# Kernel tuning notes

Measured on AMD Instinct MI355X. Metric: run time of the kernel, lower is better.

## Reference

```python
import jax, jax.numpy as jnp
import numpy as np
from jax.scipy.linalg import expm

N_MODES, N_LAYERS, CUTOFF, BATCH = 6, 6, 3, 1024
M2 = N_MODES * (N_MODES - 1) // 2                  # beamsplitter thetas per interferometer
N_IF = N_MODES * (N_MODES - 1) + (N_MODES - 1)     # interferometer param count = 35

_np_a = np.diag(np.sqrt(np.arange(1, CUTOFF)), 1)  # truncated annihilation operator
A = jnp.asarray(_np_a, jnp.complex64)
AD = A.conj().T
NVEC = jnp.arange(CUTOFF, dtype=jnp.float32)       # number operator diagonal
X_OP = A + AD                                      # x quadrature (hbar=2, PennyLane/SF convention)
BS_GEN = jnp.kron(AD, A) - jnp.kron(A, AD)         # Beamsplitter(theta, 0) generator
SQ_GEN = A @ A - AD @ AD                           # Squeezing(r, 0) generator (times r/2)
D_GEN = AD - A                                     # Displacement(r, 0) generator

def disp_gate(r):
    return expm(r.astype(jnp.complex64) * D_GEN)

def sq_gate(r):
    return expm(0.5 * r.astype(jnp.complex64) * SQ_GEN)

def bs_gate(theta):
    return expm(theta.astype(jnp.complex64) * BS_GEN)

def apply_1(psi, U, m):
    # psi: (B, D, ..., D); apply DxD gate U on mode m
    psi = jnp.moveaxis(psi, 1 + m, -1)
    psi = psi @ U.T
    return jnp.moveaxis(psi, -1, 1 + m)

def apply_1_batched(psi, U, m):
    # U: (B, D, D) per-sample gate (data-encoding displacement)
    psi = jnp.moveaxis(psi, 1 + m, -1)
    psi = jnp.einsum('b...j,bij->b...i', psi, U)
    return jnp.moveaxis(psi, -1, 1 + m)

def apply_2(psi, U, m):
    psi = jnp.moveaxis(psi, (1 + m, 2 + m), (-2, -1))
    sh = psi.shape
    psi = (psi.reshape(sh[:-2] + (CUTOFF * CUTOFF,)) @ U.T).reshape(sh)
    return jnp.moveaxis(psi, (-2, -1), (1 + m, 2 + m))

def apply_diag(psi, d, m):
    shape = [1] * psi.ndim
    shape[1 + m] = CUTOFF
    return psi * d.reshape(shape)

def interferometer(psi, params):
    theta = params[:M2]
    rphi = params[-N_MODES:]  # faithful to source: overlaps last (unused) phi param
    n = 0
    for l in range(N_MODES):
        for k in range(N_MODES - 1):
            if (l + k) % 2 != 1:
                psi = apply_2(psi, bs_gate(theta[n]), k)
                n += 1
    for i in range(max(1, N_MODES - 1)):
        psi = apply_diag(psi, jnp.exp(1j * rphi[i] * NVEC), i)
    return psi

def cv_forward(x, theta_1, theta_2, squeezing_r, displacement_r, kerr_params):
    B = x.shape[0]
    psi = jnp.zeros((B,) + (CUTOFF,) * N_MODES, jnp.complex64)
    psi = psi.at[(slice(None),) + (0,) * N_MODES].set(1.0)  # |0...0> vacuum
    for m in range(N_MODES):  # data-encoding displacements, per-sample gates
        psi = apply_1_batched(psi, jax.vmap(disp_gate)(x[:, m]), m)
    for L in range(N_LAYERS):
        psi = interferometer(psi, theta_1[L])
        for m in range(N_MODES):
            psi = apply_1(psi, sq_gate(squeezing_r[L, m] * 0.5), m)
        psi = interferometer(psi, theta_2[L])
        for m in range(N_MODES):
            psi = apply_1(psi, disp_gate(displacement_r[L, m]), m)
            psi = apply_diag(psi, jnp.exp(1j * (kerr_params[L, m] * 0.001) * NVEC * NVEC), m)
    sum_axes = tuple(range(1, psi.ndim))
    outs = [jnp.sum(jnp.conj(psi) * apply_1(psi, X_OP, m), axis=sum_axes).real
            for m in range(N_MODES)]
    return jnp.stack(outs, axis=1)  # (B, N_MODES)

def setup_inputs() -> dict:
    key = jax.random.key(0)
    ks = jax.random.split(key, 6)
    passive_sd = 0.01 * np.pi
    return {
        'x': jax.random.normal(ks[0], (BATCH, N_MODES), jnp.float32),
        'theta_1': jax.random.normal(ks[1], (N_LAYERS, N_IF), jnp.float32) * passive_sd,
        'theta_2': jax.random.normal(ks[2], (N_LAYERS, N_IF), jnp.float32) * np.float32(0.2 * np.pi),
        'squeezing_r': jax.random.normal(ks[3], (N_LAYERS, N_MODES), jnp.float32) * 1e-3,
        'displacement_r': jax.random.normal(ks[4], (N_LAYERS, N_MODES), jnp.float32) * 1e-3,
        'kerr_params': jax.random.normal(ks[5], (N_LAYERS, N_MODES), jnp.float32) * 1e-3,
    }

def reference(x, theta_1, theta_2, squeezing_r, displacement_r, kerr_params):
    return cv_forward(x, theta_1, theta_2, squeezing_r, displacement_r, kerr_params)
```

## Files before the change

kernel.cpp:

```cpp
#include <hip/hip_runtime.h>

#define SQRT2f 1.41421356237309515f
#define SQRT3f 1.73205080756887729f

__device__ __forceinline__ float2 cmul(float2 a, float2 b) {
  return make_float2(a.x*b.x - a.y*b.y, a.x*b.y + a.y*b.x);
}
__device__ __forceinline__ float2 cadd(float2 a, float2 b) {
  return make_float2(a.x + b.x, a.y + b.y);
}

__device__ __forceinline__ void bs_q(float2* q, float c, float s,
                                     float c2, float s2, float cc, float ss,
                                     float rcs) {
  float2 a1=q[1], a3=q[3], a2=q[2], a4=q[4], a6=q[6], a5=q[5], a7=q[7];
  q[1] = make_float2(c*a1.x - s*a3.x, c*a1.y - s*a3.y);
  q[3] = make_float2(s*a1.x + c*a3.x, s*a1.y + c*a3.y);
  q[2] = make_float2(cc*a2.x - rcs*a4.x + ss*a6.x, cc*a2.y - rcs*a4.y + ss*a6.y);
  q[4] = make_float2(rcs*a2.x + c2*a4.x - rcs*a6.x, rcs*a2.y + c2*a4.y - rcs*a6.y);
  q[6] = make_float2(ss*a2.x + rcs*a4.x + cc*a6.x, ss*a2.y + rcs*a4.y + cc*a6.y);
  q[5] = make_float2(c2*a5.x - s2*a7.x, c2*a5.y - s2*a7.y);
  q[7] = make_float2(s2*a5.x + c2*a7.x, s2*a5.y + c2*a7.y);
}

template<int SP>
__device__ __forceinline__ void bs_nonet(float2* __restrict__ psi, int base,
                                         float2 cs) {
  const float c = cs.x, s = cs.y;
  const float c2 = c*c - s*s, s2 = 2.f*c*s;
  const float cc = c*c, ss = s*s, rcs = SQRT2f*c*s;
  float2 a1 = psi[base+SP],   a3 = psi[base+3*SP];
  float2 a2 = psi[base+2*SP], a4 = psi[base+4*SP], a6 = psi[base+6*SP];
  float2 a5 = psi[base+5*SP], a7 = psi[base+7*SP];
  psi[base+SP]   = make_float2(c*a1.x - s*a3.x, c*a1.y - s*a3.y);
  psi[base+3*SP] = make_float2(s*a1.x + c*a3.x, s*a1.y + c*a3.y);
  psi[base+2*SP] = make_float2(cc*a2.x - rcs*a4.x + ss*a6.x,
                               cc*a2.y - rcs*a4.y + ss*a6.y);
  psi[base+4*SP] = make_float2(rcs*a2.x + c2*a4.x - rcs*a6.x,
                               rcs*a2.y + c2*a4.y - rcs*a6.y);
  psi[base+6*SP] = make_float2(ss*a2.x + rcs*a4.x + cc*a6.x,
                               ss*a2.y + rcs*a4.y + cc*a6.y);
  psi[base+5*SP] = make_float2(c2*a5.x - s2*a7.x, c2*a5.y - s2*a7.y);
  psi[base+7*SP] = make_float2(s2*a5.x + c2*a7.x, s2*a5.y + c2*a7.y);
}

template<int SP>
__device__ __forceinline__ void sqbs_nonet(float2* __restrict__ psi, int base,
                                           const float2* __restrict__ G,
                                           float2 cs) {
  const float c = cs.x, s = cs.y;
  const float c2 = c*c - s*s, s2 = 2.f*c*s;
  const float cc = c*c, ss = s*s, rcs = SQRT2f*c*s;
  float2 A00=G[0],A02=G[1],A11=G[2],A20=G[3],A22=G[4];
  float2 B00=G[5],B02=G[6],B11=G[7],B20=G[8],B22=G[9];
  float2 v[3][3];
#pragma unroll
  for (int j = 0; j < 3; ++j)
#pragma unroll
    for (int jb = 0; jb < 3; ++jb) v[j][jb] = psi[base + j*3*SP + jb*SP];
  float2 q[9];
  {
    float2 t[3][3];
#pragma unroll
    for (int j = 0; j < 3; ++j) {
      t[j][0] = cadd(cmul(B00,v[j][0]), cmul(B02,v[j][2]));
      t[j][1] = cmul(B11,v[j][1]);
      t[j][2] = cadd(cmul(B20,v[j][0]), cmul(B22,v[j][2]));
    }
#pragma unroll
    for (int ib = 0; ib < 3; ++ib) {
      q[ib]   = cadd(cmul(A00,t[0][ib]), cmul(A02,t[2][ib]));
      q[3+ib] = cmul(A11,t[1][ib]);
      q[6+ib] = cadd(cmul(A20,t[0][ib]), cmul(A22,t[2][ib]));
    }
  }
  bs_q(q, c, s, c2, s2, cc, ss, rcs);
#pragma unroll
  for (int i = 0; i < 9; ++i) psi[base + (i/3)*3*SP + (i%3)*SP] = q[i];
}

template<int SP>
__device__ __forceinline__ void dpbs_nonet(float2* __restrict__ psi, int base,
                                           const float2* __restrict__ G,
                                           float2 cs) {
  const float c = cs.x, s = cs.y;
  const float c2 = c*c - s*s, s2 = 2.f*c*s;
  const float cc = c*c, ss = s*s, rcs = SQRT2f*c*s;
  const float2* A = G; const float2* B = G + 9;
  float2 v[3][3];
#pragma unroll
  for (int j = 0; j < 3; ++j)
#pragma unroll
    for (int jb = 0; jb < 3; ++jb) v[j][jb] = psi[base + j*3*SP + jb*SP];
  float2 q[9];
  {
    float2 t[3][3];
#pragma unroll
    for (int j = 0; j < 3; ++j)
#pragma unroll
      for (int ib = 0; ib < 3; ++ib)
        t[j][ib] = cadd(cadd(cmul(B[ib*3+0],v[j][0]), cmul(B[ib*3+1],v[j][1])),
                        cmul(B[ib*3+2],v[j][2]));
#pragma unroll
    for (int i = 0; i < 3; ++i)
#pragma unroll
      for (int ib = 0; ib < 3; ++ib)
        q[i*3+ib] = cadd(cadd(cmul(A[i*3+0],t[0][ib]), cmul(A[i*3+1],t[1][ib])),
                         cmul(A[i*3+2],t[2][ib]));
  }
  bs_q(q, c, s, c2, s2, cc, ss, rcs);
#pragma unroll
  for (int i = 0; i < 9; ++i) psi[base + (i/3)*3*SP + (i%3)*SP] = q[i];
}

template<int ST, int FOLD>
__device__ __forceinline__ void cube_sweep(float2* __restrict__ psi, int base,
                                           const float2* __restrict__ G,
                                           float2 csM, float2 csH) {
  float2 v[27];
#pragma unroll
  for (int r = 0; r < 27; ++r) v[r] = psi[base + ST*r];
  if (FOLD == 1) {
    float2 A00=G[0],A02=G[1],A11=G[2],A20=G[3],A22=G[4];
    float2 B00=G[5],B02=G[6],B11=G[7],B20=G[8],B22=G[9];
#pragma unroll
    for (int t = 0; t < 9; ++t) {
      float2 u0=v[t*3], u2=v[t*3+2];
      v[t*3]   = cadd(cmul(B00,u0), cmul(B02,u2));
      v[t*3+1] = cmul(B11, v[t*3+1]);
      v[t*3+2] = cadd(cmul(B20,u0), cmul(B22,u2));
    }
#pragma unroll
    for (int h = 0; h < 3; ++h)
#pragma unroll
      for (int lo = 0; lo < 3; ++lo) {
        int rb = h*9 + lo;
        float2 u0=v[rb], u2=v[rb+6];
        v[rb]   = cadd(cmul(A00,u0), cmul(A02,u2));
        v[rb+3] = cmul(A11, v[rb+3]);
        v[rb+6] = cadd(cmul(A20,u0), cmul(A22,u2));
      }
  }
  if (FOLD == 2) {
#pragma unroll
    for (int t = 0; t < 9; ++t) {
      float2 u0=v[t*3], u1=v[t*3+1], u2=v[t*3+2];
      v[t*3]   = cadd(cadd(cmul(G[9+0],u0),cmul(G[9+1],u1)),cmul(G[9+2],u2));
      v[t*3+1] = cadd(cadd(cmul(G[9+3],u0),cmul(G[9+4],u1)),cmul(G[9+5],u2));
      v[t*3+2] = cadd(cadd(cmul(G[9+6],u0),cmul(G[9+7],u1)),cmul(G[9+8],u2));
    }
#pragma unroll
    for (int h = 0; h < 3; ++h)
#pragma unroll
      for (int lo = 0; lo < 3; ++lo) {
        int rb = h*9 + lo;
        float2 u0=v[rb], u1=v[rb+3], u2=v[rb+6];
        v[rb]   = cadd(cadd(cmul(G[0],u0),cmul(G[1],u1)),cmul(G[2],u2));
        v[rb+3] = cadd(cadd(cmul(G[3],u0),cmul(G[4],u1)),cmul(G[5],u2));
        v[rb+6] = cadd(cadd(cmul(G[6],u0),cmul(G[7],u1)),cmul(G[8],u2));
      }
  }
  {
    const float c=csM.x, s=csM.y;
    const float c2=c*c-s*s, s2=2.f*c*s, cc=c*c, ss=s*s, rcs=SQRT2f*c*s;
#pragma unroll
    for (int h = 0; h < 3; ++h) bs_q(&v[h*9], c, s, c2, s2, cc, ss, rcs);
  }
  {
    const float c=csH.x, s=csH.y;
    const float c2=c*c-s*s, s2=2.f*c*s, cc=c*c, ss=s*s, rcs=SQRT2f*c*s;
#pragma unroll
    for (int lo = 0; lo < 3; ++lo) {
      float2 q[9];
#pragma unroll
      for (int j = 0; j < 9; ++j) q[j] = v[(j/3)*9 + (j%3)*3 + lo];
      bs_q(q, c, s, c2, s2, cc, ss, rcs);
#pragma unroll
      for (int j = 0; j < 9; ++j) v[(j/3)*9 + (j%3)*3 + lo] = q[j];
    }
  }
#pragma unroll
  for (int r = 0; r < 27; ++r) psi[base + ST*r] = v[r];
}

#define BASE5(g, s0,s1,s2,s3,s4) ({ int _d=(g); int _b=(_d%3)*(s0); _d/=3; \
  _b += (_d%3)*(s1); _d/=3; _b += (_d%3)*(s2); _d/=3; _b += (_d%3)*(s3); _d/=3; \
  _b += (_d%3)*(s4); _b; })

__device__ __forceinline__ float2 dpk_entry(const float* __restrict__ dr,
                                            const float* __restrict__ th2,
                                            const float* __restrict__ kp,
                                            int L, int mode, int i, int j) {
  float sn, cn; sincosf(SQRT3f*dr[L*6+mode], &sn, &cn);
  float sw = sn*(1.f/SQRT3f), cw = (1.f-cn)*(1.f/3.f);
  float U;
  if      (i==0) U = (j==0) ? (1.f-cw)     : (j==1) ? (-sw)         : (SQRT2f*cw);
  else if (i==1) U = (j==0) ? (sw)         : (j==1) ? (1.f-3.f*cw)  : (-SQRT2f*sw);
  else           U = (j==0) ? (SQRT2f*cw)  : (j==1) ? (SQRT2f*sw)   : (1.f-2.f*cw);
  float2 ph = make_float2(1.f, 0.f);
  if (mode < 5) { float ps, pc; sincosf(th2[L*35+29+mode], &ps, &pc);
                  ph = make_float2(pc, ps); }
  float2 phj = (j==0) ? make_float2(1.f,0.f) : (j==1) ? ph : cmul(ph, ph);
  float ks, kc; sincosf(0.001f*kp[L*6+mode], &ks, &kc);
  float2 k1 = make_float2(kc, ks);
  float2 ki = (i==0) ? make_float2(1.f,0.f)
            : (i==1) ? k1 : cmul(cmul(k1,k1), cmul(k1,k1));
  float2 t = cmul(phj, ki);
  return make_float2(U*t.x, U*t.y);
}

__global__ __launch_bounds__(128)
void cvnn_kernel(const float* __restrict__ x,
                 const float* __restrict__ th1,
                 const float* __restrict__ th2,
                 const float* __restrict__ sr,
                 const float* __restrict__ dr,
                 const float* __restrict__ kp,
                 float* __restrict__ out) {
  __shared__ float2 psi[729];
  __shared__ float2 gtab[690];
  __shared__ float red[12];

  const int tid = threadIdx.x;
  const int bidx = blockIdx.x;

  for (int f = tid; f < 690; f += 128) {
    float sn, cn; float2 v;
    if (f < 180) {
      int Lp = f/15, pos = f%15;
      int L = Lp/2, pass = Lp%2;
      float th = (pass ? th2 : th1)[L*35 + pos];
      sincosf(th, &sn, &cn); v = make_float2(cn, sn);
    } else if (f < 360) {
      int i = f - 180; int Lc = i/10, e = i%10;
      int L = Lc/3, c3 = Lc%3;
      int mode = 2*c3 + (e >= 5); int ee = e%5;
      float Sq, Cq; sincosf(0.25f*SQRT2f*sr[L*6+mode], &Sq, &Cq);
      float2 ph = make_float2(1.f, 0.f);
      if (mode < 5) { float ps, pc; sincosf(th1[L*35+29+mode], &ps, &pc);
                      ph = make_float2(pc, ps); }
      float2 ph2 = cmul(ph, ph);
      if      (ee == 0) v = make_float2(Cq, 0.f);
      else if (ee == 1) v = make_float2(Sq*ph2.x, Sq*ph2.y);
      else if (ee == 2) v = ph;
      else if (ee == 3) v = make_float2(-Sq, 0.f);
      else              v = make_float2(Cq*ph2.x, Cq*ph2.y);
    } else if (f < 630) {
      int i = f - 360; int Ld = i/18, e = i%18;
      int Ls = Ld/3, c3 = Ld%3;
      int mode = 2*c3 + (e >= 9); int ee = e%9;
      v = dpk_entry(dr, th2, kp, Ls, mode, ee/3, ee%3);
    } else if (f < 684) {
      int i = f - 630; int m = i/9, e = i%9;
      int ii = e/3, jj = e%3;
      float2 D0i = dpk_entry(dr, th2, kp, 5, m, 0, ii);
      float2 D1i = dpk_entry(dr, th2, kp, 5, m, 1, ii);
      float2 D2i = dpk_entry(dr, th2, kp, 5, m, 2, ii);
      float2 D0j = dpk_entry(dr, th2, kp, 5, m, 0, jj);
      float2 D1j = dpk_entry(dr, th2, kp, 5, m, 1, jj);
      float2 D2j = dpk_entry(dr, th2, kp, 5, m, 2, jj);
      float2 c0 = make_float2(D0i.x, -D0i.y);
      float2 c1 = make_float2(D1i.x, -D1i.y);
      float2 c2 = make_float2(D2i.x, -D2i.y);
      float2 acc = cmul(c0, D1j);
      float2 tmp = make_float2(D0j.x + SQRT2f*D2j.x, D0j.y + SQRT2f*D2j.y);
      acc = cadd(acc, cmul(c1, tmp));
      acc = cadd(acc, cmul(c2, make_float2(SQRT2f*D1j.x, SQRT2f*D1j.y)));
      v = acc;
    } else {
      int mode = f - 684;
      sincosf(SQRT3f*x[bidx*6 + mode], &sn, &cn);
      v = make_float2(sn*(1.f/SQRT3f), (1.f-cn)*(1.f/3.f));
    }
    gtab[f] = v;
  }
  __syncthreads();

  for (int idx = tid; idx < 729; idx += 128) {
    float pr = 1.f; int d = idx;
#pragma unroll
    for (int mm = 5; mm >= 0; --mm) {
      int n = d % 3; d /= 3;
      float2 dc = gtab[684 + mm];
      pr *= (n==0) ? (1.f-dc.y) : (n==1) ? dc.x : SQRT2f*dc.y;
    }
    psi[idx] = make_float2(pr, 0.f);
  }

  const int g = (tid < 81) ? tid : 0;
  const int b0 = g;
  const int h = (tid < 27) ? tid : 0;
  const int n0h = h/9, hm = (h%9)/3, hl = h%3;
  const int base123 = n0h*243 + hm*3 + hl;
  const int base345 = n0h*243 + hm*81 + hl*27;
  __syncthreads();

#define W81_BS(GI)      { if (tid < 81) bs_nonet<81>(psi, b0, gtab[GI]); \
    __syncthreads(); }
#define W81_SQBS(GS,GI) { if (tid < 81) sqbs_nonet<81>(psi, b0, &gtab[GS], gtab[GI]); \
    __syncthreads(); }
#define W81_DPBS(GD,GI) { if (tid < 81) dpbs_nonet<81>(psi, b0, &gtab[GD], gtab[GI]); \
    __syncthreads(); }
#define W27_123(F,GP,GI1,GI2) { if (tid < 27) \
    cube_sweep<9,F>(psi, base123, GP, gtab[GI1], gtab[GI2]); __syncthreads(); }
#define W27_345(F,GP,GI1,GI2) { if (tid < 27) \
    cube_sweep<1,F>(psi, base345, GP, gtab[GI1], gtab[GI2]); __syncthreads(); }

#pragma unroll
  for (int L = 0; L < 6; ++L) {
    {
      const int PB = (L*2)*15;
      if (L == 0) {
        W81_BS(PB+0);
        W27_123(0, (const float2*)nullptr, PB+1, PB+3);
        W27_345(0, (const float2*)nullptr, PB+2, PB+4);
      } else {
        const int gd = 360 + (L-1)*54;
        W81_DPBS(gd+0, PB+0);
        W27_123(2, &gtab[gd+18], PB+1, PB+3);
        W27_345(2, &gtab[gd+36], PB+2, PB+4);
      }
      W81_BS(PB+5);
      W27_123(0, (const float2*)nullptr, PB+6, PB+8);
      W27_345(0, (const float2*)nullptr, PB+7, PB+9);
      W81_BS(PB+10);
      W27_123(0, (const float2*)nullptr, PB+11, PB+13);
      W27_345(0, (const float2*)nullptr, PB+12, PB+14);
    }
    {
      const int PB = (L*2+1)*15, gs = 180 + L*30;
      W81_SQBS(gs+0, PB+0);
      W27_123(1, &gtab[gs+10], PB+1, PB+3);
      W27_345(1, &gtab[gs+20], PB+2, PB+4);
      W81_BS(PB+5);
      W27_123(0, (const float2*)nullptr, PB+6, PB+8);
      W27_345(0, (const float2*)nullptr, PB+7, PB+9);
      W81_BS(PB+10);
      W27_123(0, (const float2*)nullptr, PB+11, PB+13);
      W27_345(0, (const float2*)nullptr, PB+12, PB+14);
    }
  }

  float xs[6] = {0.f,0.f,0.f,0.f,0.f,0.f};
  for (int it = 0; it < 2; ++it) {
    int t = tid + (it << 7);
    if (t < 243) {
#define XACC(m, SS, BB) { int b_ = (BB); \
      const float2* M_ = &gtab[630 + (m)*9]; \
      float d0 = M_[0].x, d1 = M_[4].x, d2 = M_[8].x; \
      float2 M01 = M_[1], M02 = M_[2], M12 = M_[5]; \
      float2 a_ = psi[b_]; float2 e_ = psi[b_+(SS)]; float2 f_ = psi[b_+2*(SS)]; \
      xs[m] += d0*(a_.x*a_.x + a_.y*a_.y) + d1*(e_.x*e_.x + e_.y*e_.y) \
             + d2*(f_.x*f_.x + f_.y*f_.y) \
        + 2.f*(M01.x*(a_.x*e_.x + a_.y*e_.y) - M01.y*(a_.x*e_.y - a_.y*e_.x)) \
        + 2.f*(M02.x*(a_.x*f_.x + a_.y*f_.y) - M02.y*(a_.x*f_.y - a_.y*f_.x)) \
        + 2.f*(M12.x*(e_.x*f_.x + e_.y*f_.y) - M12.y*(e_.x*f_.y - e_.y*f_.x)); }
      XACC(0, 243, BASE5(t, 1, 3, 9, 27, 81));
      XACC(1, 81,  BASE5(t, 1, 3, 9, 27, 243));
      XACC(2, 27,  BASE5(t, 1, 3, 9, 81, 243));
      XACC(3, 9,   BASE5(t, 1, 3, 27, 81, 243));
      XACC(4, 3,   BASE5(t, 1, 9, 27, 81, 243));
      XACC(5, 1,   BASE5(t, 3, 9, 27, 81, 243));
    }
  }
  const int lane = tid & 63, wid = tid >> 6;
#pragma unroll
  for (int m = 0; m < 6; ++m) {
    float v = xs[m];
    for (int off = 32; off > 0; off >>= 1) v += __shfl_down(v, off);
    if (lane == 0) red[wid*6 + m] = v;
  }
  __syncthreads();
  if (tid < 6) out[bidx*6 + tid] = red[tid] + red[6 + tid];
}

extern "C" void kernel_launch(void* const* d_in, const int* in_sizes, int n_in,
                              void* d_out, int out_size, void* d_ws, size_t ws_size,
                              hipStream_t stream) {
  const float* x  = (const float*)d_in[0];
  const float* t1 = (const float*)d_in[1];
  const float* t2 = (const float*)d_in[2];
  const float* sr = (const float*)d_in[3];
  const float* dr = (const float*)d_in[4];
  const float* kp = (const float*)d_in[5];
  const int B = in_sizes[0] / 6;
  cvnn_kernel<<<B, 128, 0, stream>>>(x, t1, t2, sr, dr, kp, (float*)d_out);
}
```

Baseline: 109.1 us.

## Split cube sweeps across 81 threads with cross-lane shuffles for the third mode

Each 27-element cube sweep, previously done by 27 threads each holding 27 amplitudes, is now split so that 81 threads each hold 9 amplitudes. The second beamsplitter's mode axis is exchanged between lane triples with __shfl instead of staying within one thread. This raises the parallelism in these phases and cuts per-thread register pressure and serial work. In exchange it adds shuffle traffic and spreads the active lanes over two wavefronts, with the cube index mapping done by lane arithmetic.

```diff
diff --git a/kernel.cpp b/kernel.cpp
--- a/kernel.cpp
+++ b/kernel.cpp
@@ -10,9 +10,10 @@
   return make_float2(a.x + b.x, a.y + b.y);
 }
 
-__device__ __forceinline__ void bs_q(float2* q, float c, float s,
-                                     float c2, float s2, float cc, float ss,
-                                     float rcs) {
+__device__ __forceinline__ void bs_q(float2* q, float2 cs) {
+  const float c = cs.x, s = cs.y;
+  const float c2 = c*c - s*s, s2 = 2.f*c*s;
+  const float cc = c*c, ss = s*s, rcs = SQRT2f*c*s;
   float2 a1=q[1], a3=q[3], a2=q[2], a4=q[4], a6=q[6], a5=q[5], a7=q[7];
   q[1] = make_float2(c*a1.x - s*a3.x, c*a1.y - s*a3.y);
   q[3] = make_float2(s*a1.x + c*a3.x, s*a1.y + c*a3.y);
@@ -48,9 +49,6 @@
 __device__ __forceinline__ void sqbs_nonet(float2* __restrict__ psi, int base,
                                            const float2* __restrict__ G,
                                            float2 cs) {
-  const float c = cs.x, s = cs.y;
-  const float c2 = c*c - s*s, s2 = 2.f*c*s;
-  const float cc = c*c, ss = s*s, rcs = SQRT2f*c*s;
   float2 A00=G[0],A02=G[1],A11=G[2],A20=G[3],A22=G[4];
   float2 B00=G[5],B02=G[6],B11=G[7],B20=G[8],B22=G[9];
   float2 v[3][3];
@@ -74,7 +72,7 @@
       q[6+ib] = cadd(cmul(A20,t[0][ib]), cmul(A22,t[2][ib]));
     }
   }
-  bs_q(q, c, s, c2, s2, cc, ss, rcs);
+  bs_q(q, cs);
 #pragma unroll
   for (int i = 0; i < 9; ++i) psi[base + (i/3)*3*SP + (i%3)*SP] = q[i];
 }
@@ -83,9 +81,6 @@
 __device__ __forceinline__ void dpbs_nonet(float2* __restrict__ psi, int base,
                                            const float2* __restrict__ G,
                                            float2 cs) {
-  const float c = cs.x, s = cs.y;
-  const float c2 = c*c - s*s, s2 = 2.f*c*s;
-  const float cc = c*c, ss = s*s, rcs = SQRT2f*c*s;
   const float2* A = G; const float2* B = G + 9;
   float2 v[3][3];
 #pragma unroll
@@ -108,79 +103,78 @@
         q[i*3+ib] = cadd(cadd(cmul(A[i*3+0],t[0][ib]), cmul(A[i*3+1],t[1][ib])),
                          cmul(A[i*3+2],t[2][ib]));
   }
-  bs_q(q, c, s, c2, s2, cc, ss, rcs);
+  bs_q(q, cs);
 #pragma unroll
   for (int i = 0; i < 9; ++i) psi[base + (i/3)*3*SP + (i%3)*SP] = q[i];
 }
 
-template<int ST, int FOLD>
-__device__ __forceinline__ void cube_sweep(float2* __restrict__ psi, int base,
-                                           const float2* __restrict__ G,
-                                           float2 csM, float2 csH) {
-  float2 v[27];
-#pragma unroll
-  for (int r = 0; r < 27; ++r) v[r] = psi[base + ST*r];
+template<int FOLD, int SH, int SM, int SL>
+__device__ __forceinline__ void cube81(float2* __restrict__ psi, int base,
+                                       int h, int lb3,
+                                       const float2* __restrict__ G,
+                                       float2 csM, float2 csH) {
+  float2 v[9];
+#pragma unroll
+  for (int m = 0; m < 3; ++m)
+#pragma unroll
+    for (int l = 0; l < 3; ++l) v[m*3+l] = psi[base + h*SH + m*SM + l*SL];
   if (FOLD == 1) {
     float2 A00=G[0],A02=G[1],A11=G[2],A20=G[3],A22=G[4];
     float2 B00=G[5],B02=G[6],B11=G[7],B20=G[8],B22=G[9];
 #pragma unroll
-    for (int t = 0; t < 9; ++t) {
-      float2 u0=v[t*3], u2=v[t*3+2];
-      v[t*3]   = cadd(cmul(B00,u0), cmul(B02,u2));
-      v[t*3+1] = cmul(B11, v[t*3+1]);
-      v[t*3+2] = cadd(cmul(B20,u0), cmul(B22,u2));
-    }
-#pragma unroll
-    for (int h = 0; h < 3; ++h)
-#pragma unroll
-      for (int lo = 0; lo < 3; ++lo) {
-        int rb = h*9 + lo;
-        float2 u0=v[rb], u2=v[rb+6];
-        v[rb]   = cadd(cmul(A00,u0), cmul(A02,u2));
-        v[rb+3] = cmul(A11, v[rb+3]);
-        v[rb+6] = cadd(cmul(A20,u0), cmul(A22,u2));
-      }
+    for (int m = 0; m < 3; ++m) {
+      float2 u0=v[m*3], u2=v[m*3+2];
+      v[m*3]   = cadd(cmul(B00,u0), cmul(B02,u2));
+      v[m*3+1] = cmul(B11, v[m*3+1]);
+      v[m*3+2] = cadd(cmul(B20,u0), cmul(B22,u2));
+    }
+#pragma unroll
+    for (int l = 0; l < 3; ++l) {
+      float2 u0=v[l], u2=v[6+l];
+      v[l]   = cadd(cmul(A00,u0), cmul(A02,u2));
+      v[3+l] = cmul(A11, v[3+l]);
+      v[6+l] = cadd(cmul(A20,u0), cmul(A22,u2));
+    }
   }
   if (FOLD == 2) {
 #pragma unroll
-    for (int t = 0; t < 9; ++t) {
-      float2 u0=v[t*3], u1=v[t*3+1], u2=v[t*3+2];
-      v[t*3]   = cadd(cadd(cmul(G[9+0],u0),cmul(G[9+1],u1)),cmul(G[9+2],u2));
-      v[t*3+1] = cadd(cadd(cmul(G[9+3],u0),cmul(G[9+4],u1)),cmul(G[9+5],u2));
-      v[t*3+2] = cadd(cadd(cmul(G[9+6],u0),cmul(G[9+7],u1)),cmul(G[9+8],u2));
-    }
-#pragma unroll
-    for (int h = 0; h < 3; ++h)
-#pragma unroll
-      for (int lo = 0; lo < 3; ++lo) {
-        int rb = h*9 + lo;
-        float2 u0=v[rb], u1=v[rb+3], u2=v[rb+6];
-        v[rb]   = cadd(cadd(cmul(G[0],u0),cmul(G[1],u1)),cmul(G[2],u2));
-        v[rb+3] = cadd(cadd(cmul(G[3],u0),cmul(G[4],u1)),cmul(G[5],u2));
-        v[rb+6] = cadd(cadd(cmul(G[6],u0),cmul(G[7],u1)),cmul(G[8],u2));
-      }
-  }
-  {
-    const float c=csM.x, s=csM.y;
-    const float c2=c*c-s*s, s2=2.f*c*s, cc=c*c, ss=s*s, rcs=SQRT2f*c*s;
-#pragma unroll
-    for (int h = 0; h < 3; ++h) bs_q(&v[h*9], c, s, c2, s2, cc, ss, rcs);
-  }
-  {
-    const float c=csH.x, s=csH.y;
-    const float c2=c*c-s*s, s2=2.f*c*s, cc=c*c, ss=s*s, rcs=SQRT2f*c*s;
-#pragma unroll
-    for (int lo = 0; lo < 3; ++lo) {
-      float2 q[9];
-#pragma unroll
-      for (int j = 0; j < 9; ++j) q[j] = v[(j/3)*9 + (j%3)*3 + lo];
-      bs_q(q, c, s, c2, s2, cc, ss, rcs);
-#pragma unroll
-      for (int j = 0; j < 9; ++j) v[(j/3)*9 + (j%3)*3 + lo] = q[j];
-    }
-  }
-#pragma unroll
-  for (int r = 0; r < 27; ++r) psi[base + ST*r] = v[r];
+    for (int m = 0; m < 3; ++m) {
+      float2 u0=v[m*3], u1=v[m*3+1], u2=v[m*3+2];
+      v[m*3]   = cadd(cadd(cmul(G[9+0],u0),cmul(G[9+1],u1)),cmul(G[9+2],u2));
+      v[m*3+1] = cadd(cadd(cmul(G[9+3],u0),cmul(G[9+4],u1)),cmul(G[9+5],u2));
+      v[m*3+2] = cadd(cadd(cmul(G[9+6],u0),cmul(G[9+7],u1)),cmul(G[9+8],u2));
+    }
+#pragma unroll
+    for (int l = 0; l < 3; ++l) {
+      float2 u0=v[l], u1=v[3+l], u2=v[6+l];
+      v[l]   = cadd(cadd(cmul(G[0],u0),cmul(G[1],u1)),cmul(G[2],u2));
+      v[3+l] = cadd(cadd(cmul(G[3],u0),cmul(G[4],u1)),cmul(G[5],u2));
+      v[6+l] = cadd(cadd(cmul(G[6],u0),cmul(G[7],u1)),cmul(G[8],u2));
+    }
+  }
+  bs_q(v, csM);
+  const int hp1 = (h==2) ? 0 : h+1;
+  const int hp2 = (h==0) ? 2 : h-1;
+  const int l1 = lb3 + hp1, l2 = lb3 + hp2;
+  float2 a[9];
+#pragma unroll
+  for (int m = 0; m < 3; ++m) {
+    float2 own = (h==0) ? v[3*m]   : (h==1) ? v[3*m+1] : v[3*m+2];
+    float2 e1  = (h==0) ? v[3*m+2] : (h==1) ? v[3*m]   : v[3*m+1];
+    float2 e2  = (h==0) ? v[3*m+1] : (h==1) ? v[3*m+2] : v[3*m];
+    float2 r1, r2;
+    r1.x = __shfl(e1.x, l1, 64); r1.y = __shfl(e1.y, l1, 64);
+    r2.x = __shfl(e2.x, l2, 64); r2.y = __shfl(e2.y, l2, 64);
+    a[0+m] = (h==0) ? own : (h==2) ? r1 : r2;
+    a[3+m] = (h==1) ? own : (h==0) ? r1 : r2;
+    a[6+m] = (h==2) ? own : (h==1) ? r1 : r2;
+  }
+  bs_q(a, csH);
+#pragma unroll
+  for (int hi = 0; hi < 3; ++hi)
+#pragma unroll
+    for (int m = 0; m < 3; ++m)
+      psi[base + hi*SH + m*SM + h*SL] = a[3*hi+m];
 }
 
 #define BASE5(g, s0,s1,s2,s3,s4) ({ int _d=(g); int _b=(_d%3)*(s0); _d/=3; \
@@ -289,10 +283,15 @@
 
   const int g = (tid < 81) ? tid : 0;
   const int b0 = g;
-  const int h = (tid < 27) ? tid : 0;
-  const int n0h = h/9, hm = (h%9)/3, hl = h%3;
-  const int base123 = n0h*243 + hm*3 + hl;
-  const int base345 = n0h*243 + hm*81 + hl*27;
+  const int lane = tid & 63, wv = tid >> 6;
+  const bool cact = (wv == 0) ? (lane < 63) : (lane < 18);
+  const int lc = lane / 3;
+  const int cc = (wv == 0) ? lc : (21 + lc);
+  const int ch = lane % 3;
+  const int lb3 = lc * 3;
+  const int q0 = cc/9, q1 = (cc%9)/3, q2 = cc%3;
+  const int cbase123 = q0*243 + q1*3 + q2;
+  const int cbase345 = q0*243 + q1*81 + q2*27;
   __syncthreads();
 
 #define W81_BS(GI)      { if (tid < 81) bs_nonet<81>(psi, b0, gtab[GI]); \
@@ -301,10 +300,12 @@
     __syncthreads(); }
 #define W81_DPBS(GD,GI) { if (tid < 81) dpbs_nonet<81>(psi, b0, &gtab[GD], gtab[GI]); \
     __syncthreads(); }
-#define W27_123(F,GP,GI1,GI2) { if (tid < 27) \
-    cube_sweep<9,F>(psi, base123, GP, gtab[GI1], gtab[GI2]); __syncthreads(); }
-#define W27_345(F,GP,GI1,GI2) { if (tid < 27) \
-    cube_sweep<1,F>(psi, base345, GP, gtab[GI1], gtab[GI2]); __syncthreads(); }
+#define C123(F,GP,GIM,GIH) { if (cact) \
+    cube81<F,81,27,9>(psi, cbase123, ch, lb3, GP, gtab[GIM], gtab[GIH]); \
+    __syncthreads(); }
+#define C345(F,GP,GIM,GIH) { if (cact) \
+    cube81<F,9,3,1>(psi, cbase345, ch, lb3, GP, gtab[GIM], gtab[GIH]); \
+    __syncthreads(); }
 
 #pragma unroll
   for (int L = 0; L < 6; ++L) {
@@ -312,32 +313,32 @@
       const int PB = (L*2)*15;
       if (L == 0) {
         W81_BS(PB+0);
-        W27_123(0, (const float2*)nullptr, PB+1, PB+3);
-        W27_345(0, (const float2*)nullptr, PB+2, PB+4);
+        C123(0, (const float2*)nullptr, PB+1, PB+3);
+        C345(0, (const float2*)nullptr, PB+2, PB+4);
       } else {
         const int gd = 360 + (L-1)*54;
         W81_DPBS(gd+0, PB+0);
-        W27_123(2, &gtab[gd+18], PB+1, PB+3);
-        W27_345(2, &gtab[gd+36], PB+2, PB+4);
+        C123(2, &gtab[gd+18], PB+1, PB+3);
+        C345(2, &gtab[gd+36], PB+2, PB+4);
       }
       W81_BS(PB+5);
-      W27_123(0, (const float2*)nullptr, PB+6, PB+8);
-      W27_345(0, (const float2*)nullptr, PB+7, PB+9);
+      C123(0, (const float2*)nullptr, PB+6, PB+8);
+      C345(0, (const float2*)nullptr, PB+7, PB+9);
       W81_BS(PB+10);
-      W27_123(0, (const float2*)nullptr, PB+11, PB+13);
-      W27_345(0, (const float2*)nullptr, PB+12, PB+14);
+      C123(0, (const float2*)nullptr, PB+11, PB+13);
+      C345(0, (const float2*)nullptr, PB+12, PB+14);
     }
     {
       const int PB = (L*2+1)*15, gs = 180 + L*30;
       W81_SQBS(gs+0, PB+0);
-      W27_123(1, &gtab[gs+10], PB+1, PB+3);
-      W27_345(1, &gtab[gs+20], PB+2, PB+4);
+      C123(1, &gtab[gs+10], PB+1, PB+3);
+      C345(1, &gtab[gs+20], PB+2, PB+4);
       W81_BS(PB+5);
-      W27_123(0, (const float2*)nullptr, PB+6, PB+8);
-      W27_345(0, (const float2*)nullptr, PB+7, PB+9);
+      C123(0, (const float2*)nullptr, PB+6, PB+8);
+      C345(0, (const float2*)nullptr, PB+7, PB+9);
       W81_BS(PB+10);
-      W27_123(0, (const float2*)nullptr, PB+11, PB+13);
-      W27_345(0, (const float2*)nullptr, PB+12, PB+14);
+      C123(0, (const float2*)nullptr, PB+11, PB+13);
+      C345(0, (const float2*)nullptr, PB+12, PB+14);
     }
   }
 
@@ -363,12 +364,12 @@
       XACC(5, 1,   BASE5(t, 3, 9, 27, 81, 243));
     }
   }
-  const int lane = tid & 63, wid = tid >> 6;
+  const int wid = tid >> 6;
 #pragma unroll
   for (int m = 0; m < 6; ++m) {
     float v = xs[m];
     for (int off = 32; off > 0; off >>= 1) v += __shfl_down(v, off);
-    if (lane == 0) red[wid*6 + m] = v;
+    if ((tid & 63) == 0) red[wid*6 + m] = v;
   }
   __syncthreads();
   if (tid < 6) out[bidx*6 + tid] = red[tid] + red[6 + tid];
```

New measurement: 156.8 us. 43.7% more time.
